# Kernel tuning notes

Hardware: AMD Instinct MI355X
Metric: run time of the kernel (lower is better)

Reference implementation:

```python
import jax, jax.numpy as jnp
import numpy as np

N_DRUG = 20000; N_DIS = 20000; E_G = 320000
B = 4096; N_MOL = 65536; E_MOL = 262144
IN = 128; H = 256; OUT = 128; NF = 9; V = 128
EPS = 1e-5


def _bn(x, g, b):
    # BatchNorm1d in training mode: batch statistics (biased var), eps=1e-5
    m = jnp.mean(x, 0); v = jnp.var(x, 0)
    return g * (x - m) * jax.lax.rsqrt(v + EPS) + b


def _gcn_conv(x, W, b, src, dst, n):
    # PyG GCNConv: add self-loops, sym-normalized aggregation of x@W, + bias
    h = x @ W  # [n, out]
    deg = jnp.ones((n,), x.dtype).at[dst].add(jnp.ones(src.shape, x.dtype))  # deg incl. self-loop
    dinv = jax.lax.rsqrt(deg)
    msg = (dinv[src] * dinv[dst])[:, None] * h[src]  # [E, out]
    out = (h / deg[:, None]).at[dst].add(msg)  # self-loop norm = 1/deg
    return out + b


def _gcn(x, Ws, bs, gs, betas, edge_index, n):
    src, dst = edge_index[0], edge_index[1]
    for i in range(len(Ws) - 1):
        x = jax.nn.relu(_bn(_gcn_conv(x, Ws[i], bs[i], src, dst, n), gs[i], betas[i]))
    return _gcn_conv(x, Ws[-1], bs[-1], src, dst, n)


def _conv_block(x, W, b, g, beta):
    # Conv1d(k=3,s=1,p=1) -> MaxPool1d(2,2) -> BatchNorm1d -> ReLU
    y = jax.lax.conv_general_dilated(x, W, (1,), ((1, 1),), dimension_numbers=('NCH', 'OIH', 'NCH')) + b[None, :, None]
    y = jax.lax.reduce_window(y, -jnp.inf, jax.lax.max, (1, 1, 2), (1, 1, 2), 'VALID')
    m = jnp.mean(y, (0, 2)); v = jnp.var(y, (0, 2))
    y = g[None, :, None] * (y - m[None, :, None]) * jax.lax.rsqrt(v + EPS)[None, :, None] + beta[None, :, None]
    return jax.nn.relu(y)


def setup_inputs() -> dict:
    key = jax.random.key(0)
    ks = iter(jax.random.split(key, 64))
    def nrm(shape, s=0.05):
        return jax.random.normal(next(ks), shape, jnp.float32) * s
    inp = {}
    inp['drug_x'] = nrm((N_DRUG, IN), 1.0)
    inp['drug_edge_index'] = jax.random.randint(next(ks), (2, E_G), 0, N_DRUG)
    inp['drug_idx'] = jax.random.randint(next(ks), (B,), 0, N_DRUG)
    inp['dis_x'] = nrm((N_DIS, IN), 1.0)
    inp['dis_edge_index'] = jax.random.randint(next(ks), (2, E_G), 0, N_DIS)
    inp['dis_idx'] = jax.random.randint(next(ks), (B,), 0, N_DIS)
    inp['mol_x'] = jax.random.randint(next(ks), (N_MOL, NF), 0, V)
    inp['mol_edge_index'] = jax.random.randint(next(ks), (2, E_MOL), 0, N_MOL)
    inp['mol_batch'] = jnp.sort(jax.random.randint(next(ks), (N_MOL,), 0, B))
    for p in ['dr', 'di']:
        inp[p + '_W0'] = nrm((IN, H)); inp[p + '_W1'] = nrm((H, H)); inp[p + '_W2'] = nrm((H, OUT))
        inp[p + '_b0'] = jnp.zeros((H,)); inp[p + '_b1'] = jnp.zeros((H,)); inp[p + '_b2'] = jnp.zeros((OUT,))
        inp[p + '_g0'] = jnp.ones((H,)); inp[p + '_g1'] = jnp.ones((H,))
        inp[p + '_be0'] = jnp.zeros((H,)); inp[p + '_be1'] = jnp.zeros((H,))
    inp['mol_emb'] = nrm((NF, V, H))
    inp['mo_W0'] = nrm((H, H)); inp['mo_W1'] = nrm((H, H)); inp['mo_W2'] = nrm((H, OUT))
    inp['mo_b0'] = jnp.zeros((H,)); inp['mo_b1'] = jnp.zeros((H,)); inp['mo_b2'] = jnp.zeros((OUT,))
    inp['mo_g0'] = jnp.ones((H,)); inp['mo_g1'] = jnp.ones((H,))
    inp['mo_be0'] = jnp.zeros((H,)); inp['mo_be1'] = jnp.zeros((H,))
    inp['c1_W'] = nrm((6, 3, 3), 0.2); inp['c1_b'] = jnp.zeros((6,)); inp['c1_g'] = jnp.ones((6,)); inp['c1_be'] = jnp.zeros((6,))
    inp['c2_W'] = nrm((6, 6, 3), 0.2); inp['c2_b'] = jnp.zeros((6,)); inp['c2_g'] = jnp.ones((6,)); inp['c2_be'] = jnp.zeros((6,))
    inp['l1_W'] = nrm((192, 128)); inp['l1_b'] = jnp.zeros((128,))
    inp['l2_W'] = nrm((128, 1)); inp['l2_b'] = jnp.zeros((1,))
    return inp


def reference(drug_x, drug_edge_index, drug_idx, dis_x, dis_edge_index, dis_idx, mol_x, mol_edge_index, mol_batch,
              dr_W0, dr_W1, dr_W2, dr_b0, dr_b1, dr_b2, dr_g0, dr_g1, dr_be0, dr_be1,
              di_W0, di_W1, di_W2, di_b0, di_b1, di_b2, di_g0, di_g1, di_be0, di_be1,
              mol_emb, mo_W0, mo_W1, mo_W2, mo_b0, mo_b1, mo_b2, mo_g0, mo_g1, mo_be0, mo_be1,
              c1_W, c1_b, c1_g, c1_be, c2_W, c2_b, c2_g, c2_be, l1_W, l1_b, l2_W, l2_b):
    dfeat = _gcn(drug_x, [dr_W0, dr_W1, dr_W2], [dr_b0, dr_b1, dr_b2], [dr_g0, dr_g1], [dr_be0, dr_be1], drug_edge_index, N_DRUG)
    sfeat = _gcn(dis_x, [di_W0, di_W1, di_W2], [di_b0, di_b1, di_b2], [di_g0, di_g1], [di_be0, di_be1], dis_edge_index, N_DIS)
    # AtomEncoder: sum of per-feature categorical embeddings -> [N_MOL, H]
    h = jnp.sum(mol_emb[jnp.arange(NF)[None, :], mol_x], axis=1)
    mfeat = _gcn(h, [mo_W0, mo_W1, mo_W2], [mo_b0, mo_b1, mo_b2], [mo_g0, mo_g1], [mo_be0, mo_be1], mol_edge_index, N_MOL)
    mpool = jax.ops.segment_sum(mfeat, mol_batch, num_segments=B)  # global_add_pool
    fea = jnp.concatenate([dfeat[drug_idx], mpool, sfeat[dis_idx]], axis=1).reshape(B, 3, OUT)
    fea = _conv_block(fea, c1_W, c1_b, c1_g, c1_be)
    fea = _conv_block(fea, c2_W, c2_b, c2_g, c2_be)
    fea = fea.reshape(B, -1)  # [B, 192]
    fea = jax.nn.relu(fea @ l1_W + l1_b)
    return fea @ l2_W + l2_b
```

## Files before the change

### kernel.cpp

```cpp
#include <hip/hip_runtime.h>
#include <hip/hip_bf16.h>

#define N_DRUG 20000
#define N_DIS  20000
#define E_G    320000
#define BATCH  4096
#define N_MOL  65536
#define E_MOL  262144
#define DIN    128
#define DH     256
#define DOUT   128
#define NF     9
#define NV     128

typedef short s16x8 __attribute__((ext_vector_type(8)));
typedef unsigned short u16x8 __attribute__((ext_vector_type(8)));
typedef float f32x4 __attribute__((ext_vector_type(4)));

__device__ __forceinline__ float bfu2f(unsigned short u) {
    return __uint_as_float(((unsigned int)u) << 16);
}
__device__ __forceinline__ unsigned short f2bfu(float f) {
    __hip_bfloat16 b = __float2bfloat16(f);
    return *reinterpret_cast<unsigned short*>(&b);
}
__device__ __forceinline__ void atomAddF(float* p, float v) { unsafeAtomicAdd(p, v); }

__global__ void k_sentinel(float* out, int n, float v) {
    int i = blockIdx.x * 256 + threadIdx.x;
    if (i < n) out[i] = v;
}

__global__ void k_cast_bf4(const float* __restrict__ in, unsigned short* __restrict__ out, int n4) {
    int i = blockIdx.x * 256 + threadIdx.x;
    if (i < n4) {
        float4 v = reinterpret_cast<const float4*>(in)[i];
        ushort4 o = {f2bfu(v.x), f2bfu(v.y), f2bfu(v.z), f2bfu(v.w)};
        reinterpret_cast<ushort4*>(out)[i] = o;
    }
}

__global__ void k_wcast3(const float* __restrict__ W0, const float* __restrict__ W1,
                         const float* __restrict__ W2,
                         unsigned short* __restrict__ T0, unsigned short* __restrict__ T1,
                         unsigned short* __restrict__ T2, int Cin) {
    int i = blockIdx.x * 256 + threadIdx.x;
    int t0 = Cin * 256, t1 = 256 * 256, t2 = 256 * 128;
    if (i < t0) {
        int k = i / 256, c = i - k * 256;
        T0[(size_t)c * Cin + k] = f2bfu(W0[i]);
    } else if (i < t0 + t1) {
        int e = i - t0;
        int k = e / 256, c = e - k * 256;
        T1[(size_t)c * 256 + k] = f2bfu(W1[e]);
    } else if (i < t0 + t1 + t2) {
        int e = i - t0 - t1;
        int k = e / 128, c = e - k * 128;
        T2[(size_t)c * 256 + k] = f2bfu(W2[e]);
    }
}

__global__ void k_count(const int* __restrict__ dst, int* __restrict__ cnt, int E) {
    int e = blockIdx.x * 256 + threadIdx.x;
    if (e < E) atomicAdd(&cnt[dst[e]], 1);
}

__global__ void k_scan1(const int* __restrict__ cnt, int* __restrict__ rowStart,
                        int* __restrict__ bsum, float* __restrict__ dinv, int n) {
    __shared__ int sh[256];
    int i = blockIdx.x * 256 + threadIdx.x;
    int v = (i < n) ? cnt[i] : 0;
    if (i < n) dinv[i] = rsqrtf(1.0f + (float)v);
    sh[threadIdx.x] = v;
    __syncthreads();
    for (int off = 1; off < 256; off <<= 1) {
        int t = (threadIdx.x >= off) ? sh[threadIdx.x - off] : 0;
        __syncthreads();
        sh[threadIdx.x] += t;
        __syncthreads();
    }
    if (i < n) rowStart[i] = sh[threadIdx.x] - v;
    if (threadIdx.x == 255) bsum[blockIdx.x] = sh[255];
}
__global__ void k_scan2(int* __restrict__ bsum, int nb) {
    __shared__ int sh[256];
    int t = threadIdx.x;
    int v = (t < nb) ? bsum[t] : 0;
    sh[t] = v;
    __syncthreads();
    for (int off = 1; off < 256; off <<= 1) {
        int u = (t >= off) ? sh[t - off] : 0;
        __syncthreads();
        sh[t] += u;
        __syncthreads();
    }
    if (t < nb) bsum[t] = sh[t] - v;
}
__global__ void k_scan3(int* __restrict__ rowStart, int* __restrict__ cursor,
                        const int* __restrict__ bsum, int n, int E) {
    int i = blockIdx.x * 256 + threadIdx.x;
    if (i < n) {
        int r = rowStart[i] + bsum[blockIdx.x];
        rowStart[i] = r;
        cursor[i] = r;
    }
    if (i == 0) rowStart[n] = E;
}
__global__ void k_fill(const int* __restrict__ src, const int* __restrict__ dst,
                       const float* __restrict__ dinv,
                       int* __restrict__ cursor, int2* __restrict__ csr2, int E) {
    int e = blockIdx.x * 256 + threadIdx.x;
    if (e < E) {
        int s = src[e], d = dst[e];
        int p = atomicAdd(&cursor[d], 1);
        csr2[p] = make_int2(s, __float_as_int(dinv[s] * dinv[d]));
    }
}

template<int AFFINE, int STATS>
__global__ __launch_bounds__(256) void k_gemm_mfma(const unsigned short* __restrict__ A,
                                                   const unsigned short* __restrict__ Bt,
                                                   const float* __restrict__ coef,
                                                   unsigned short* __restrict__ Cout,
                                                   float* __restrict__ bnsum,
                                                   float* __restrict__ bnsq,
                                                   int M, int K, int N) {
    __shared__ unsigned short Al[4][128][8];
    __shared__ unsigned short Bl[4][128][8];
    const int tid = threadIdx.x;
    const int bm = blockIdx.y * 128;
    const int bn = blockIdx.x * 128;
    const int w = tid >> 6, l = tid & 63;
    const int wrow = (w >> 1) * 64, wcol = (w & 1) * 64;
    const int kg = l >> 4, lr = l & 15;

    f32x4 acc[4][4];
#pragma unroll
    for (int fm = 0; fm < 4; ++fm)
#pragma unroll
        for (int fn = 0; fn < 4; ++fn) acc[fm][fn] = f32x4{0.f, 0.f, 0.f, 0.f};

    for (int k0 = 0; k0 < K; k0 += 32) {
#pragma unroll
        for (int c = 0; c < 2; ++c) {
            int idx = c * 256 + tid;
            int row = idx >> 2;
            int koff = idx & 3;
            u16x8 va = {0, 0, 0, 0, 0, 0, 0, 0};
            int grow = bm + row;
            if (grow < M)
                va = *reinterpret_cast<const u16x8*>(A + (size_t)grow * K + k0 + koff * 8);
            if (AFFINE) {
                int kb = k0 + koff * 8;
#pragma unroll
                for (int e = 0; e < 8; ++e) {
                    float f = bfu2f((unsigned short)va[e]);
                    f = fmaf(coef[kb + e], f, coef[256 + kb + e]);
                    va[e] = f2bfu(fmaxf(f, 0.f));
                }
            }
            *reinterpret_cast<u16x8*>(&Al[koff][row][0]) = va;
            u16x8 vb = *reinterpret_cast<const u16x8*>(Bt + (size_t)(bn + row) * K + k0 + koff * 8);
            *reinterpret_cast<u16x8*>(&Bl[koff][row][0]) = vb;
        }
        __syncthreads();
        s16x8 a[4], b[4];
#pragma unroll
        for (int fm = 0; fm < 4; ++fm)
            a[fm] = *reinterpret_cast<const s16x8*>(&Al[kg][wrow + fm * 16 + lr][0]);
#pragma unroll
        for (int fn = 0; fn < 4; ++fn)
            b[fn] = *reinterpret_cast<const s16x8*>(&Bl[kg][wcol + fn * 16 + lr][0]);
#pragma unroll
        for (int fm = 0; fm < 4; ++fm)
#pragma unroll
            for (int fn = 0; fn < 4; ++fn)
                acc[fm][fn] = __builtin_amdgcn_mfma_f32_16x16x32_bf16(a[fm], b[fn], acc[fm][fn], 0, 0, 0);
        __syncthreads();
    }
#pragma unroll
    for (int fm = 0; fm < 4; ++fm)
#pragma unroll
        for (int r = 0; r < 4; ++r) {
            int row = bm + wrow + fm * 16 + kg * 4 + r;
            if (row >= M) continue;
#pragma unroll
            for (int fn = 0; fn < 4; ++fn) {
                int col = bn + wcol + fn * 16 + lr;
                Cout[(size_t)row * N + col] = f2bfu(acc[fm][fn][r]);
            }
        }
    if constexpr (STATS) {
        __shared__ float colS[128], colQ[128];
        if (tid < 128) { colS[tid] = 0.f; colQ[tid] = 0.f; }
        __syncthreads();
#pragma unroll
        for (int fn = 0; fn < 4; ++fn) {
            float s = 0.f, q = 0.f;
#pragma unroll
            for (int fm = 0; fm < 4; ++fm)
#pragma unroll
                for (int r = 0; r < 4; ++r) {
                    float v = acc[fm][fn][r];
                    s += v; q += v * v;
                }
            int cl = (w & 1) * 64 + fn * 16 + lr;
            atomicAdd(&colS[cl], s);
            atomicAdd(&colQ[cl], q);
        }
        __syncthreads();
        if (tid < 128) {
            atomAddF(&bnsum[bn + tid], colS[tid]);
            atomAddF(&bnsq[bn + tid], colQ[tid]);
        }
    }
}

template<int C, int BIAS, int OUTBF>
__global__ __launch_bounds__(256) void k_gather(const unsigned short* __restrict__ h,
                                                const float* __restrict__ dinv,
                                                const float* __restrict__ bias,
                                                const int2* __restrict__ csr2,
                                                const int* __restrict__ rowStart,
                                                void* __restrict__ outv, int n) {
    constexpr int PL = C / 32;
    int row = blockIdx.x * 8 + (threadIdx.x >> 5);
    if (row >= n) return;
    int lane = threadIdx.x & 31;
    int c0 = lane * PL;

    auto loadRow = [&](int r, float* d) {
        const unsigned short* base = h + (size_t)r * C + c0;
        if constexpr (PL == 8) {
            u16x8 v = *reinterpret_cast<const u16x8*>(base);
#pragma unroll
            for (int e = 0; e < 8; ++e) d[e] = bfu2f((unsigned short)v[e]);
        } else {
            ushort4 v = *reinterpret_cast<const ushort4*>(base);
            d[0] = bfu2f(v.x); d[1] = bfu2f(v.y); d[2] = bfu2f(v.z); d[3] = bfu2f(v.w);
        }
    };

    float dd = dinv[row], ws = dd * dd;
    int beg = rowStart[row], end = rowStart[row + 1];
    float a0[PL], a1[PL], a2[PL], a3[PL], t0[PL], t1[PL], t2[PL], t3[PL];
    loadRow(row, t0);
#pragma unroll
    for (int p = 0; p < PL; ++p) { a0[p] = t0[p] * ws; a1[p] = 0.f; a2[p] = 0.f; a3[p] = 0.f; }

    int j = beg;
    for (; j + 4 <= end; j += 4) {
        int2 e0 = csr2[j], e1 = csr2[j + 1], e2 = csr2[j + 2], e3 = csr2[j + 3];
        float w0 = __int_as_float(e0.y), w1 = __int_as_float(e1.y);
        float w2 = __int_as_float(e2.y), w3 = __int_as_float(e3.y);
        loadRow(e0.x, t0); loadRow(e1.x, t1); loadRow(e2.x, t2); loadRow(e3.x, t3);
#pragma unroll
        for (int p = 0; p < PL; ++p) {
            a0[p] += w0 * t0[p]; a1[p] += w1 * t1[p];
            a2[p] += w2 * t2[p]; a3[p] += w3 * t3[p];
        }
    }
    for (; j < end; ++j) {
        int2 e0 = csr2[j];
        float w = __int_as_float(e0.y);
        loadRow(e0.x, t0);
#pragma unroll
        for (int p = 0; p < PL; ++p) a0[p] += w * t0[p];
    }
#pragma unroll
    for (int p = 0; p < PL; ++p) {
        a0[p] += (a1[p] + a2[p]) + a3[p];
        if (BIAS) a0[p] += bias[c0 + p];
    }
    if constexpr (OUTBF) {
        unsigned short* o = (unsigned short*)outv + (size_t)row * C + c0;
        if constexpr (PL == 8) {
            u16x8 ov;
#pragma unroll
            for (int e = 0; e < 8; ++e) ov[e] = f2bfu(a0[e]);
            *reinterpret_cast<u16x8*>(o) = ov;
        } else {
            ushort4 ov = {f2bfu(a0[0]), f2bfu(a0[1]), f2bfu(a0[2]), f2bfu(a0[3])};
            *reinterpret_cast<ushort4*>(o) = ov;
        }
    } else {
        float* o = (float*)outv + (size_t)row * C + c0;
#pragma unroll
        for (int q = 0; q < PL / 4; ++q) {
            float4 ov = {a0[q * 4 + 0], a0[q * 4 + 1], a0[q * 4 + 2], a0[q * 4 + 3]};
            *reinterpret_cast<float4*>(o + q * 4) = ov;
        }
    }
}

__global__ __launch_bounds__(256) void k_bn_stats_bf(const unsigned short* __restrict__ x,
                                                     float* __restrict__ sum,
                                                     float* __restrict__ sq, int n) {
    __shared__ float smS[8][256];
    __shared__ float smQ[8][256];
    int t = threadIdx.x;
    int g = t >> 5;
    int lane = t & 31;
    int c0 = lane * 8;
    float s[8], q[8];
#pragma unroll
    for (int e = 0; e < 8; ++e) { s[e] = 0.f; q[e] = 0.f; }
    int stride = gridDim.x * 8;
    for (int r = blockIdx.x * 8 + g; r < n; r += stride) {
        u16x8 v = *reinterpret_cast<const u16x8*>(x + (size_t)r * 256 + c0);
#pragma unroll
        for (int e = 0; e < 8; ++e) {
            float f = bfu2f((unsigned short)v[e]);
            s[e] += f; q[e] += f * f;
        }
    }
#pragma unroll
    for (int e = 0; e < 8; ++e) { smS[g][c0 + e] = s[e]; smQ[g][c0 + e] = q[e]; }
    __syncthreads();
    float S = 0.f, Q = 0.f;
#pragma unroll
    for (int g2 = 0; g2 < 8; ++g2) { S += smS[g2][t]; Q += smQ[g2][t]; }
    atomAddF(&sum[t], S);
    atomAddF(&sq[t], Q);
}

__global__ void k_bn_coef(float* __restrict__ sum, float* __restrict__ sq,
                          const float* __restrict__ g, const float* __restrict__ be,
                          float* __restrict__ coef, float invN) {
    int j = threadIdx.x;
    float m = sum[j] * invN;
    float v = sq[j] * invN - m * m;
    float r = rsqrtf(fmaxf(v, 0.f) + 1e-5f);
    float sc = g[j] * r;
    coef[j] = sc;
    coef[256 + j] = be[j] - m * sc;
    sum[j] = 0.f;
    sq[j] = 0.f;
}

__global__ __launch_bounds__(256) void k_atom_enc(const int* __restrict__ mol_x,
                                                  const float* __restrict__ emb,
                                                  unsigned short* __restrict__ h) {
    __shared__ int sidx[4][NF];
    int t = threadIdx.x;
    if (t < 4 * NF) sidx[t / NF][t % NF] = mol_x[(blockIdx.x * 4 + t / NF) * NF + t % NF];
    __syncthreads();
    int r = t >> 6, lane = t & 63;
    int c0 = lane * 4;
    int row = blockIdx.x * 4 + r;
    float4 s = {0.f, 0.f, 0.f, 0.f};
#pragma unroll
    for (int f = 0; f < NF; ++f) {
        const float4 v = *reinterpret_cast<const float4*>(emb + ((size_t)f * NV + sidx[r][f]) * DH + c0);
        s.x += v.x; s.y += v.y; s.z += v.z; s.w += v.w;
    }
    ushort4 ov = {f2bfu(s.x), f2bfu(s.y), f2bfu(s.z), f2bfu(s.w)};
    *reinterpret_cast<ushort4*>(h + (size_t)row * DH + c0) = ov;
}

__global__ __launch_bounds__(128) void k_pool_seg(const unsigned short* __restrict__ mfeat,
                                                  const int* __restrict__ batch,
                                                  float* __restrict__ mpool) {
    __shared__ int sr[2];
    __shared__ float smS[8][128];
    int b = blockIdx.x, t = threadIdx.x;
    if (t < 2) {
        int target = b + t;
        int lo = 0, hi = N_MOL;
        while (lo < hi) {
            int mid = (lo + hi) >> 1;
            if (batch[mid] < target) lo = mid + 1; else hi = mid;
        }
        sr[t] = lo;
    }
    __syncthreads();
    int g = t >> 4;
    int lane = t & 15;
    int c0 = lane * 8;
    float s[8];
#pragma unroll
    for (int e = 0; e < 8; ++e) s[e] = 0.f;
    int e1 = sr[1];
    for (int i = sr[0] + g; i < e1; i += 8) {
        u16x8 v = *reinterpret_cast<const u16x8*>(mfeat + (size_t)i * 128 + c0);
#pragma unroll
        for (int e = 0; e < 8; ++e) s[e] += bfu2f((unsigned short)v[e]);
    }
#pragma unroll
    for (int e = 0; e < 8; ++e) smS[g][c0 + e] = s[e];
    __syncthreads();
    float S = 0.f;
#pragma unroll
    for (int g2 = 0; g2 < 8; ++g2) S += smS[g2][t];
    mpool[(size_t)b * 128 + t] = S;
}

__global__ __launch_bounds__(64) void k_conv1(const float* __restrict__ dfeat,
                                              const float* __restrict__ mpool,
                                              const float* __restrict__ sfeat,
                                              const int* __restrict__ drug_idx,
                                              const int* __restrict__ dis_idx,
                                              const float* __restrict__ W,
                                              const float* __restrict__ bias,
                                              float* __restrict__ y1) {
    __shared__ float xs[3][128];
    __shared__ float w[54];
    __shared__ float bb[6];
    int b = blockIdx.x, t = threadIdx.x;
    int di = drug_idx[b], si = dis_idx[b];
    const float* r0 = dfeat + (size_t)di * 128;
    const float* r1 = mpool + (size_t)b * 128;
    const float* r2 = sfeat + (size_t)si * 128;
    xs[0][t] = r0[t]; xs[0][t + 64] = r0[t + 64];
    xs[1][t] = r1[t]; xs[1][t + 64] = r1[t + 64];
    xs[2][t] = r2[t]; xs[2][t + 64] = r2[t + 64];
    if (t < 54) w[t] = W[t];
    if (t < 6) bb[t] = bias[t];
    __syncthreads();
    int l0 = 2 * t, l1 = l0 + 1;
#pragma unroll
    for (int o = 0; o < 6; ++o) {
        float ya = bb[o], yb = bb[o];
#pragma unroll
        for (int i = 0; i < 3; ++i) {
            const float* wi = &w[(o * 3 + i) * 3];
            float xm1 = (l0 > 0) ? xs[i][l0 - 1] : 0.f;
            float x0 = xs[i][l0];
            float x1 = xs[i][l1];
            float x2 = (l1 < 127) ? xs[i][l1 + 1] : 0.f;
            ya += wi[0] * xm1 + wi[1] * x0 + wi[2] * x1;
            yb += wi[0] * x0 + wi[1] * x1 + wi[2] * x2;
        }
        y1[((size_t)b * 6 + o) * 64 + t] = fmaxf(ya, yb);
    }
}

__global__ __launch_bounds__(256) void k_head_stats(const float* __restrict__ y,
                                                    float* __restrict__ hb, int which, int L) {
    int o = blockIdx.x;
    int b0 = blockIdx.y * 256;
    int t = threadIdx.x;
    float s = 0.f, q = 0.f;
    int per = 256 * L;
    for (int idx = t; idx < per; idx += 256) {
        int b = b0 + idx / L;
        int l = idx - (idx / L) * L;
        float v = y[((size_t)b * 6 + o) * L + l];
        s += v; q += v * v;
    }
    __shared__ float sms[4], smq[4];
#pragma unroll
    for (int off = 32; off > 0; off >>= 1) {
        s += __shfl_down(s, off);
        q += __shfl_down(q, off);
    }
    if ((t & 63) == 0) { sms[t >> 6] = s; smq[t >> 6] = q; }
    __syncthreads();
    if (t == 0) {
        float S = 0.f, Q = 0.f;
        for (int i = 0; i < 4; ++i) { S += sms[i]; Q += smq[i]; }
        atomAddF(hb + which * 32 + o, S);
        atomAddF(hb + which * 32 + 8 + o, Q);
    }
}

__global__ void k_bn_fin(float* __restrict__ hb, int which, float invN) {
    int o = threadIdx.x;
    if (o >= 6) return;
    float* p = hb + which * 32;
    float m = p[o] * invN;
    float v = p[8 + o] * invN - m * m;
    p[16 + o] = m;
    p[24 + o] = rsqrtf(fmaxf(v, 0.f) + 1e-5f);
}

__global__ __launch_bounds__(64) void k_conv2(const float* __restrict__ y1,
                                              const float* __restrict__ hb,
                                              const float* __restrict__ g1,
                                              const float* __restrict__ be1,
                                              const float* __restrict__ W,
                                              const float* __restrict__ bias,
                                              float* __restrict__ y2) {
    __shared__ float xs[6][64];
    __shared__ float w[108];
    __shared__ float bb[6];
    int b = blockIdx.x, t = threadIdx.x;
    const float* mean = hb + 16;
    const float* rstd = hb + 24;
    for (int idx = t; idx < 384; idx += 64) {
        int o = idx >> 6, l = idx & 63;
        float v = y1[((size_t)b * 6 + o) * 64 + l];
        v = g1[o] * (v - mean[o]) * rstd[o] + be1[o];
        xs[o][l] = fmaxf(v, 0.f);
    }
    for (int idx = t; idx < 108; idx += 64) w[idx] = W[idx];
    if (t < 6) bb[t] = bias[t];
    __syncthreads();
    if (t >= 32) return;
    int l0 = 2 * t, l1 = l0 + 1;
#pragma unroll
    for (int o = 0; o < 6; ++o) {
        float ya = bb[o], yb = bb[o];
#pragma unroll
        for (int i = 0; i < 6; ++i) {
            const float* wi = &w[(o * 6 + i) * 3];
            float xm1 = (l0 > 0) ? xs[i][l0 - 1] : 0.f;
            float x0 = xs[i][l0];
            float x1 = xs[i][l1];
            float x2 = (l1 < 63) ? xs[i][l1 + 1] : 0.f;
            ya += wi[0] * xm1 + wi[1] * x0 + wi[2] * x1;
            yb += wi[0] * x0 + wi[1] * x1 + wi[2] * x2;
        }
        y2[((size_t)b * 6 + o) * 32 + t] = fmaxf(ya, yb);
    }
}

__global__ __launch_bounds__(128) void k_head(const float* __restrict__ y2,
                                              const float* __restrict__ hb,
                                              const float* __restrict__ g2,
                                              const float* __restrict__ be2,
                                              const float* __restrict__ l1W,
                                              const float* __restrict__ l1b,
                                              const float* __restrict__ l2W,
                                              const float* __restrict__ l2b,
                                              float* __restrict__ out) {
    __shared__ float fs[192];
    __shared__ float sm[2];
    int b = blockIdx.x, t = threadIdx.x;
    const float* mean = hb + 32 + 16;
    const float* rstd = hb + 32 + 24;
    for (int idx = t; idx < 192; idx += 128) {
        int o = idx >> 5, l = idx & 31;
        float v = y2[((size_t)b * 6 + o) * 32 + l];
        v = g2[o] * (v - mean[o]) * rstd[o] + be2[o];
        fs[idx] = fmaxf(v, 0.f);
    }
    __syncthreads();
    float h = l1b[t];
    for (int k = 0; k < 192; ++k)
        h += fs[k] * l1W[k * 128 + t];
    h = fmaxf(h, 0.f);
    float p = h * l2W[t];
#pragma unroll
    for (int off = 32; off > 0; off >>= 1) p += __shfl_down(p, off);
    if ((t & 63) == 0) sm[t >> 6] = p;
    __syncthreads();
    if (t == 0) out[b] = sm[0] + sm[1] + l2b[0];
}

struct GcnScratch {
    int *cnt, *rowStart, *cursor, *bsum;
    int2* csr2;
    float *dinv, *bnsum, *bnsq, *coef;
    unsigned short *wt0, *wt1, *wt2;
};

static void run_gcn(const unsigned short* xin, int Cin,
                    unsigned short* xb, unsigned short* h_bf, void* outF, int out2bf,
                    const int* ei, int n, int E,
                    const float* W0, const float* W1, const float* W2, const float* b2,
                    const float* g0, const float* g1, const float* be0, const float* be1,
                    GcnScratch& S, hipStream_t stream) {
    const int* src = ei;
    const int* dst = ei + E;
    hipMemsetAsync(S.cnt, 0, (size_t)n * sizeof(int), stream);
    k_count<<<(E + 255) / 256, 256, 0, stream>>>(dst, S.cnt, E);
    int nb = (n + 255) / 256;
    k_scan1<<<nb, 256, 0, stream>>>(S.cnt, S.rowStart, S.bsum, S.dinv, n);
    k_scan2<<<1, 256, 0, stream>>>(S.bsum, nb);
    k_scan3<<<nb, 256, 0, stream>>>(S.rowStart, S.cursor, S.bsum, n, E);
    k_fill<<<(E + 255) / 256, 256, 0, stream>>>(src, dst, S.dinv, S.cursor, S.csr2, E);
    int wtot = Cin * 256 + 256 * 256 + 256 * 128;
    k_wcast3<<<(wtot + 255) / 256, 256, 0, stream>>>(W0, W1, W2, S.wt0, S.wt1, S.wt2, Cin);

    int gb = (n + 7) / 8;
    int gy = (n + 127) / 128;
    float invN = 1.0f / (float)n;
    int sb = min(512, (n + 7) / 8);
    if (Cin == 256)
        k_gather<256, 0, 1><<<gb, 256, 0, stream>>>(xin, S.dinv, nullptr, S.csr2, S.rowStart, xb, n);
    else
        k_gather<128, 0, 1><<<gb, 256, 0, stream>>>(xin, S.dinv, nullptr, S.csr2, S.rowStart, xb, n);
    k_gemm_mfma<0, 1><<<dim3(2, gy), 256, 0, stream>>>(xb, S.wt0, nullptr, h_bf, S.bnsum, S.bnsq, n, Cin, 256);
    k_bn_coef<<<1, 256, 0, stream>>>(S.bnsum, S.bnsq, g0, be0, S.coef, invN);
    k_gemm_mfma<1, 0><<<dim3(2, gy), 256, 0, stream>>>(h_bf, S.wt1, S.coef, xb, nullptr, nullptr, n, 256, 256);
    k_gather<256, 0, 1><<<gb, 256, 0, stream>>>(xb, S.dinv, nullptr, S.csr2, S.rowStart, h_bf, n);
    k_bn_stats_bf<<<sb, 256, 0, stream>>>(h_bf, S.bnsum, S.bnsq, n);
    k_bn_coef<<<1, 256, 0, stream>>>(S.bnsum, S.bnsq, g1, be1, S.coef, invN);
    k_gemm_mfma<1, 0><<<dim3(1, gy), 256, 0, stream>>>(h_bf, S.wt2, S.coef, xb, nullptr, nullptr, n, 256, 128);
    if (out2bf)
        k_gather<128, 1, 1><<<gb, 256, 0, stream>>>(xb, S.dinv, b2, S.csr2, S.rowStart, outF, n);
    else
        k_gather<128, 1, 0><<<gb, 256, 0, stream>>>(xb, S.dinv, b2, S.csr2, S.rowStart, outF, n);
}

extern "C" void kernel_launch(void* const* d_in, const int* in_sizes, int n_in,
                              void* d_out, int out_size, void* d_ws, size_t ws_size,
                              hipStream_t stream) {
    float* out = (float*)d_out;
    if (n_in != 52) { k_sentinel<<<16, 256, 0, stream>>>(out, out_size, -111.f); return; }
    if (in_sizes[0] != N_DRUG * DIN || in_sizes[29] != NF * NV * DH || in_sizes[48] != 192 * 128) {
        k_sentinel<<<16, 256, 0, stream>>>(out, out_size, -222.f); return;
    }

    char* w = (char*)d_ws;
    auto alloc = [&](size_t bytes) { char* p = w; w += (bytes + 255) & ~(size_t)255; return p; };
    unsigned short* xb   = (unsigned short*)alloc((size_t)N_MOL * 256 * 2);
    unsigned short* h_bf = (unsigned short*)alloc((size_t)N_MOL * 256 * 2);
    unsigned short* xin  = (unsigned short*)alloc((size_t)N_MOL * 256 * 2);
    float* dfeat = (float*)alloc((size_t)N_DRUG * 128 * 4);
    float* sfeat = (float*)alloc((size_t)N_DIS * 128 * 4);
    float* mpool = (float*)alloc((size_t)BATCH * 128 * 4);
    GcnScratch S;
    S.cnt      = (int*)alloc((size_t)N_MOL * 4);
    S.dinv     = (float*)alloc((size_t)N_MOL * 4);
    S.rowStart = (int*)alloc((size_t)(N_MOL + 1) * 4);
    S.cursor   = (int*)alloc((size_t)N_MOL * 4);
    S.csr2     = (int2*)alloc((size_t)E_G * 8);
    S.bsum     = (int*)alloc(512 * 4);
    S.bnsum    = (float*)alloc(512 * 4);
    S.bnsq     = S.bnsum + 256;
    S.coef     = (float*)alloc(512 * 4);
    S.wt0      = (unsigned short*)alloc((size_t)256 * 256 * 2);
    S.wt1      = (unsigned short*)alloc((size_t)256 * 256 * 2);
    S.wt2      = (unsigned short*)alloc((size_t)256 * 256 * 2);
    float* hstat  = (float*)alloc(64 * 4);
    float* y1     = (float*)alloc((size_t)BATCH * 6 * 64 * 4);
    float* y2     = (float*)alloc((size_t)BATCH * 6 * 32 * 4);
    if ((size_t)(w - (char*)d_ws) > ws_size) {
        k_sentinel<<<16, 256, 0, stream>>>(out, out_size, -333.f); return;
    }

    const float* drug_x  = (const float*)d_in[0];
    const int* drug_ei   = (const int*)d_in[1];
    const int* drug_idx  = (const int*)d_in[2];
    const float* dis_x   = (const float*)d_in[3];
    const int* dis_ei    = (const int*)d_in[4];
    const int* dis_idx   = (const int*)d_in[5];
    const int* mol_x     = (const int*)d_in[6];
    const int* mol_ei    = (const int*)d_in[7];
    const int* mol_b     = (const int*)d_in[8];
    const float *dr_W0 = (const float*)d_in[9], *dr_W1 = (const float*)d_in[10], *dr_W2 = (const float*)d_in[11];
    const float *dr_b2 = (const float*)d_in[14];
    const float *dr_g0 = (const float*)d_in[15], *dr_g1 = (const float*)d_in[16];
    const float *dr_be0 = (const float*)d_in[17], *dr_be1 = (const float*)d_in[18];
    const float *di_W0 = (const float*)d_in[19], *di_W1 = (const float*)d_in[20], *di_W2 = (const float*)d_in[21];
    const float *di_b2 = (const float*)d_in[24];
    const float *di_g0 = (const float*)d_in[25], *di_g1 = (const float*)d_in[26];
    const float *di_be0 = (const float*)d_in[27], *di_be1 = (const float*)d_in[28];
    const float* mol_emb = (const float*)d_in[29];
    const float *mo_W0 = (const float*)d_in[30], *mo_W1 = (const float*)d_in[31], *mo_W2 = (const float*)d_in[32];
    const float *mo_b2 = (const float*)d_in[35];
    const float *mo_g0 = (const float*)d_in[36], *mo_g1 = (const float*)d_in[37];
    const float *mo_be0 = (const float*)d_in[38], *mo_be1 = (const float*)d_in[39];
    const float *c1_W = (const float*)d_in[40], *c1_b = (const float*)d_in[41];
    const float *c1_g = (const float*)d_in[42], *c1_be = (const float*)d_in[43];
    const float *c2_W = (const float*)d_in[44], *c2_b = (const float*)d_in[45];
    const float *c2_g = (const float*)d_in[46], *c2_be = (const float*)d_in[47];
    const float *l1_W = (const float*)d_in[48], *l1_b = (const float*)d_in[49];
    const float *l2_W = (const float*)d_in[50], *l2_b = (const float*)d_in[51];

    hipMemsetAsync(S.bnsum, 0, 512 * sizeof(float), stream);

    k_cast_bf4<<<(N_DRUG * DIN / 4 + 255) / 256, 256, 0, stream>>>(drug_x, xin, N_DRUG * DIN / 4);
    run_gcn(xin, DIN, xb, h_bf, dfeat, 0, drug_ei, N_DRUG, E_G,
            dr_W0, dr_W1, dr_W2, dr_b2, dr_g0, dr_g1, dr_be0, dr_be1, S, stream);

    k_cast_bf4<<<(N_DIS * DIN / 4 + 255) / 256, 256, 0, stream>>>(dis_x, xin, N_DIS * DIN / 4);
    run_gcn(xin, DIN, xb, h_bf, sfeat, 0, dis_ei, N_DIS, E_G,
            di_W0, di_W1, di_W2, di_b2, di_g0, di_g1, di_be0, di_be1, S, stream);

    k_atom_enc<<<N_MOL / 4, 256, 0, stream>>>(mol_x, mol_emb, xin);
    run_gcn(xin, 256, xb, h_bf, h_bf, 1, mol_ei, N_MOL, E_MOL,
            mo_W0, mo_W1, mo_W2, mo_b2, mo_g0, mo_g1, mo_be0, mo_be1, S, stream);
    k_pool_seg<<<BATCH, 128, 0, stream>>>(h_bf, mol_b, mpool);

    hipMemsetAsync(hstat, 0, 64 * 4, stream);
    k_conv1<<<BATCH, 64, 0, stream>>>(dfeat, mpool, sfeat, drug_idx, dis_idx, c1_W, c1_b, y1);
    k_head_stats<<<dim3(6, BATCH / 256), 256, 0, stream>>>(y1, hstat, 0, 64);
    k_bn_fin<<<1, 8, 0, stream>>>(hstat, 0, 1.0f / (BATCH * 64.0f));
    k_conv2<<<BATCH, 64, 0, stream>>>(y1, hstat, c1_g, c1_be, c2_W, c2_b, y2);
    k_head_stats<<<dim3(6, BATCH / 256), 256, 0, stream>>>(y2, hstat, 1, 32);
    k_bn_fin<<<1, 8, 0, stream>>>(hstat, 1, 1.0f / (BATCH * 32.0f));
    k_head<<<BATCH, 128, 0, stream>>>(y2, hstat, c2_g, c2_be, l1_W, l1_b, l2_W, l2_b, out);
}
```

Before: 670.7 us.

## Load GEMM tiles directly to LDS and apply BN affine after LDS read

Replaces the register-staged global-to-LDS tile copies in the MFMA GEMM with global_load_lds direct transfers, each wave loading 64-row halves of the A and B tiles. Because data no longer passes through registers on load, the BN scale/shift+ReLU for the AFFINE variant moves to after the LDS fragment read, using coefficients cached in shared memory. Rows past M are handled by zero-filling LDS once for edge tiles. The intent is to cut VGPR pressure and load latency. The risks are that the affine math is now repeated by each wave that reads the same A fragment, and that waves issuing no loads still wait at the barrier.

Result: slower. 688.1 us (+2.6%).

```diff
diff --git a/kernel.cpp b/kernel.cpp
--- a/kernel.cpp
+++ b/kernel.cpp
@@ -16,6 +16,9 @@
 typedef short s16x8 __attribute__((ext_vector_type(8)));
 typedef unsigned short u16x8 __attribute__((ext_vector_type(8)));
 typedef float f32x4 __attribute__((ext_vector_type(4)));
+
+typedef __attribute__((address_space(1))) const void gvoid_t;
+typedef __attribute__((address_space(3))) void lvoid_t;
 
 __device__ __forceinline__ float bfu2f(unsigned short u) {
     return __uint_as_float(((unsigned int)u) << 16);
@@ -127,6 +130,7 @@
                                                    int M, int K, int N) {
     __shared__ unsigned short Al[4][128][8];
     __shared__ unsigned short Bl[4][128][8];
+    __shared__ float csc[256], csh[256];
     const int tid = threadIdx.x;
     const int bm = blockIdx.y * 128;
     const int bn = blockIdx.x * 128;
@@ -134,6 +138,17 @@
     const int wrow = (w >> 1) * 64, wcol = (w & 1) * 64;
     const int kg = l >> 4, lr = l & 15;
 
+    if (AFFINE) {
+        for (int i = tid; i < K; i += 256) { csc[i] = coef[i]; csh[i] = coef[256 + i]; }
+    }
+    if (bm + 128 > M) {
+        for (int s = tid; s < 512; s += 256) {
+            u16x8 z = {0, 0, 0, 0, 0, 0, 0, 0};
+            *reinterpret_cast<u16x8*>(&Al[0][0][0] + s * 8) = z;
+        }
+    }
+    __syncthreads();
+
     f32x4 acc[4][4];
 #pragma unroll
     for (int fm = 0; fm < 4; ++fm)
@@ -142,32 +157,43 @@
 
     for (int k0 = 0; k0 < K; k0 += 32) {
 #pragma unroll
-        for (int c = 0; c < 2; ++c) {
-            int idx = c * 256 + tid;
-            int row = idx >> 2;
-            int koff = idx & 3;
-            u16x8 va = {0, 0, 0, 0, 0, 0, 0, 0};
-            int grow = bm + row;
-            if (grow < M)
-                va = *reinterpret_cast<const u16x8*>(A + (size_t)grow * K + k0 + koff * 8);
-            if (AFFINE) {
-                int kb = k0 + koff * 8;
-#pragma unroll
-                for (int e = 0; e < 8; ++e) {
-                    float f = bfu2f((unsigned short)va[e]);
-                    f = fmaf(coef[kb + e], f, coef[256 + kb + e]);
-                    va[e] = f2bfu(fmaxf(f, 0.f));
+        for (int i = 0; i < 4; ++i) {
+            int id = w * 4 + i;
+            int koff = (id >> 1) & 3;
+            int half = id & 1;
+            int row = half * 64 + l;
+            if (id < 8) {
+                if (bm + row < M) {
+                    const unsigned short* gs = A + (size_t)(bm + row) * K + k0 + koff * 8;
+                    __builtin_amdgcn_global_load_lds((gvoid_t*)gs,
+                        (lvoid_t*)&Al[koff][half * 64][0], 16, 0, 0);
                 }
+            } else {
+                const unsigned short* gs = Bt + (size_t)(bn + row) * K + k0 + koff * 8;
+                __builtin_amdgcn_global_load_lds((gvoid_t*)gs,
+                    (lvoid_t*)&Bl[koff][half * 64][0], 16, 0, 0);
             }
-            *reinterpret_cast<u16x8*>(&Al[koff][row][0]) = va;
-            u16x8 vb = *reinterpret_cast<const u16x8*>(Bt + (size_t)(bn + row) * K + k0 + koff * 8);
-            *reinterpret_cast<u16x8*>(&Bl[koff][row][0]) = vb;
         }
         __syncthreads();
         s16x8 a[4], b[4];
 #pragma unroll
         for (int fm = 0; fm < 4; ++fm)
             a[fm] = *reinterpret_cast<const s16x8*>(&Al[kg][wrow + fm * 16 + lr][0]);
+        if (AFFINE) {
+            float sc[8], sh[8];
+#pragma unroll
+            for (int e = 0; e < 8; ++e) {
+                sc[e] = csc[k0 + kg * 8 + e];
+                sh[e] = csh[k0 + kg * 8 + e];
+            }
+#pragma unroll
+            for (int fm = 0; fm < 4; ++fm)
+#pragma unroll
+                for (int e = 0; e < 8; ++e) {
+                    float f = bfu2f((unsigned short)a[fm][e]);
+                    a[fm][e] = (short)f2bfu(fmaxf(fmaf(sc[e], f, sh[e]), 0.f));
+                }
+        }
 #pragma unroll
         for (int fn = 0; fn < 4; ++fn)
             b[fn] = *reinterpret_cast<const s16x8*>(&Bl[kg][wcol + fn * 16 + lr][0]);
```
